# Optimization experiments

Hardware: AMD Instinct MI355X
Metric: run time of the kernel (lower is better)

Reference implementation:

```python
import jax, jax.numpy as jnp
import numpy as np

THRESHOLD = 15.0
INIT_RATIO = 0.5
WINDOW_T = 100
C1 = INIT_RATIO * THRESHOLD            # 7.5, initial membrane potential
C2 = 1.0 / THRESHOLD                   # 1/15
C3 = (1.0 - INIT_RATIO) / WINDOW_T     # 0.005


def snn_layer(spikes, mem, hat_spikes, W, b):
    """One SNNLinear layer in training mode.
    spikes: [T,B,in], mem: [B,out], hat_spikes: [B,in], W: [out,in], b: [out].
    Returns (ss [T,B,out], mem_final [B,out], hat_s [B,out]).
    """
    T = spikes.shape[0]
    # delta_us = fc(spikes): [T,B,out]
    delta_us = jnp.einsum('tbi,oi->tbo', spikes, W) + b

    def step(carry, du):
        m, sum_u = carry
        m = m + du
        s = (m > THRESHOLD).astype(m.dtype)
        m = jnp.clip(m, 0.0, THRESHOLD)
        sum_u = sum_u + m
        m = m - m * s  # reset to 0 where spiked
        return (m, sum_u), s

    (mem_f, sum_u), ss = jax.lax.scan(step, (mem, jnp.zeros_like(mem)), delta_us)
    # In torch this loop runs under no_grad
    ss = jax.lax.stop_gradient(ss)
    mem_f = jax.lax.stop_gradient(mem_f)
    hat_s_fwd = jnp.mean(ss, axis=0)
    hat_u_fwd = jax.lax.stop_gradient(sum_u) / T

    # delta_u = fc(hat_spikes): grad path
    delta_u = hat_spikes @ W.T + b
    # ForwardFirstBackwardSecond: forward value hat_u_fwd, gradient flows to delta_u
    hat_u = hat_u_fwd + (delta_u - jax.lax.stop_gradient(delta_u))
    g = jnp.maximum(hat_u * C2, C3)
    hat_s = hat_s_fwd + (g - jax.lax.stop_gradient(g))
    return ss, mem_f, hat_s


def setup_inputs() -> dict:
    key = jax.random.key(0)
    ks = jax.random.split(key, 8)
    T, B = 50, 256
    shapes = [1024, 2048, 2048, 1024]
    spikes = jax.random.bernoulli(ks[0], 0.1, (T, B, shapes[0])).astype(jnp.float32)
    hat_spk = jax.random.uniform(ks[1], (B, shapes[0]), jnp.float32) * 0.2
    mem0 = jnp.full((B, shapes[1]), C1, jnp.float32)
    mem1 = jnp.full((B, shapes[2]), C1, jnp.float32)
    mem2 = jnp.full((B, shapes[3]), C1, jnp.float32)
    W0 = jax.random.normal(ks[2], (shapes[1], shapes[0]), jnp.float32)
    b0 = jax.random.normal(ks[3], (shapes[1],), jnp.float32)
    W1 = jax.random.normal(ks[4], (shapes[2], shapes[1]), jnp.float32)
    b1 = jax.random.normal(ks[5], (shapes[2],), jnp.float32)
    W2 = jax.random.normal(ks[6], (shapes[3], shapes[2]), jnp.float32)
    b2 = jax.random.normal(ks[7], (shapes[3],), jnp.float32)
    return {"spikes": spikes, "hat_spk": hat_spk, "mem0": mem0, "mem1": mem1,
            "mem2": mem2, "W0": W0, "b0": b0, "W1": W1, "b1": b1, "W2": W2, "b2": b2}


def reference(spikes, hat_spk, mem0, mem1, mem2, W0, b0, W1, b1, W2, b2):
    s, _, h = snn_layer(spikes, mem0, hat_spk, W0, b0)
    s, _, h = snn_layer(s, mem1, h, W1, b1)
    s, _, h = snn_layer(s, mem2, h, W2, b2)
    return s, h
```

## Files before the change

### kernel.cpp

```cpp
#include <hip/hip_runtime.h>
#include <cstdint>
#include <cstddef>

#define T_STEPS 50
#define BATCH   256
#define TC      10
#define TCG     5

__global__ __launch_bounds__(256)
void pack_spikes_k(const float* __restrict__ A, uint32_t* __restrict__ P) {
    const int i    = (int)blockIdx.x * 256 + (int)threadIdx.x;
    const int lane = (int)threadIdx.x & 63;
    const unsigned long long m = __ballot(A[i] != 0.0f);
    if ((lane & 31) == 0)
        P[i >> 5] = (uint32_t)((lane & 32) ? (m >> 32) : m);
}


template<int K, int O>
__global__ __launch_bounds__(256)
void gemm_k(const uint32_t* __restrict__ Ain,
            const float* __restrict__ W,
            const float* __restrict__ bias,
            float* __restrict__ DU)
{
    constexpr int NW = K / 32;
    __shared__ float Wsm[32][256];

    const int tid = (int)threadIdx.x;
    const int o_l = tid & 63;
    const int wid = tid >> 6;
    const int o0  = (int)blockIdx.x * 256;
    const int oq  = o0 + 4 * o_l;
    const int b_u = __builtin_amdgcn_readfirstlane((int)blockIdx.y * 4 + wid);
    const int tc0 = (int)blockIdx.z * TCG;
    const uint32_t* __restrict__ Ab = Ain + (size_t)b_u * NW;

    const float4 bb4 = *(const float4*)(bias + oq);

    float pre[TCG][4], cur[TCG][4];
#pragma unroll
    for (int tt = 0; tt < TCG; ++tt)
#pragma unroll
        for (int c = 0; c < 4; ++c) { pre[tt][c] = 0.0f; cur[tt][c] = 0.0f; }

    for (int wt = 0; wt < NW; ++wt) {
#pragma unroll
        for (int r = 0; r < 8; ++r) {
            const int i    = tid + r * 256;
            const int orow = i >> 3;
            const int q    = i & 7;
            const float4 v = *(const float4*)(W + (size_t)(o0 + orow) * K + wt * 32 + q * 4);
            const int pc   = (((orow >> 2) ^ q) << 2) | (orow & 3);
            Wsm[4 * q + 0][pc] = v.x;
            Wsm[4 * q + 1][pc] = v.y;
            Wsm[4 * q + 2][pc] = v.z;
            Wsm[4 * q + 3][pc] = v.w;
        }
        uint32_t M[TCG];
#pragma unroll
        for (int tt = 0; tt < TCG; ++tt)
            M[tt] = __builtin_amdgcn_readfirstlane(
                        Ab[(size_t)(tc0 + tt) * (BATCH * NW) + wt]);
        __syncthreads();

#pragma unroll 8
        for (int kk = 0; kk < 32; ++kk) {
            const float4 wv = *(const float4*)&Wsm[kk][(o_l ^ ((kk >> 2) & 7)) << 2];
#pragma unroll
            for (int tt = 0; tt < TCG; ++tt) {
                const uint32_t fb = ((M[tt] >> kk) & 1u) ? 0x3f800000u : 0u;
                const float f = __builtin_bit_cast(float, fb);
                cur[tt][0] = __builtin_fmaf(f, wv.x, cur[tt][0]);
                cur[tt][1] = __builtin_fmaf(f, wv.y, cur[tt][1]);
                cur[tt][2] = __builtin_fmaf(f, wv.z, cur[tt][2]);
                cur[tt][3] = __builtin_fmaf(f, wv.w, cur[tt][3]);
            }
        }
        __syncthreads();

        if (((wt + 1) & 15) == 0) {
#pragma unroll
            for (int tt = 0; tt < TCG; ++tt)
#pragma unroll
                for (int c = 0; c < 4; ++c) {
                    pre[tt][c] = pre[tt][c] + cur[tt][c];
                    cur[tt][c] = 0.0f;
                }
        }
    }

#pragma unroll
    for (int tt = 0; tt < TCG; ++tt) {
        const int t = tc0 + tt;
        float4 du;
        du.x = (pre[tt][0] + cur[tt][0]) + bb4.x;
        du.y = (pre[tt][1] + cur[tt][1]) + bb4.y;
        du.z = (pre[tt][2] + cur[tt][2]) + bb4.z;
        du.w = (pre[tt][3] + cur[tt][3]) + bb4.w;
        *(float4*)(DU + (size_t)t * (BATCH * O) + (size_t)b_u * O + oq) = du;
    }
}

template<int O, bool LAST>
__global__ __launch_bounds__(256)
void scan_k(const float* __restrict__ DU,
            const float* __restrict__ mem,
            uint32_t* __restrict__ Pout,
            float* __restrict__ SSout,
            float* __restrict__ Hout)
{
    constexpr int NWO = O / 32;
    __shared__ unsigned char pk[4][64];

    const int tid = (int)threadIdx.x;
    const int o_l = tid & 63;
    const int wid = tid >> 6;
    const int b   = (int)blockIdx.y;
    const int o0  = (int)blockIdx.x * 1024 + wid * 256;
    const int oq  = o0 + 4 * o_l;

    float4 m4 = *(const float4*)(mem + (size_t)b * O + oq);
    int c0 = 0, c1 = 0, c2 = 0, c3 = 0;

    float4 du = *(const float4*)(DU + (size_t)b * O + oq);

    for (int t = 0; t < T_STEPS; ++t) {
        float4 dun;
        if (t + 1 < T_STEPS)
            dun = *(const float4*)(DU + (size_t)(t + 1) * (BATCH * O) + (size_t)b * O + oq);
        m4.x += du.x; m4.y += du.y; m4.z += du.z; m4.w += du.w;
        const bool s0 = m4.x > 15.0f, s1 = m4.y > 15.0f,
                   s2 = m4.z > 15.0f, s3 = m4.w > 15.0f;
        m4.x = fminf(fmaxf(m4.x, 0.0f), 15.0f);
        m4.y = fminf(fmaxf(m4.y, 0.0f), 15.0f);
        m4.z = fminf(fmaxf(m4.z, 0.0f), 15.0f);
        m4.w = fminf(fmaxf(m4.w, 0.0f), 15.0f);
        if (s0) { m4.x = 0.0f; ++c0; }
        if (s1) { m4.y = 0.0f; ++c1; }
        if (s2) { m4.z = 0.0f; ++c2; }
        if (s3) { m4.w = 0.0f; ++c3; }

        if (LAST) {
            *(float4*)(SSout + (size_t)t * (BATCH * O) + (size_t)b * O + oq) =
                make_float4(s0 ? 1.0f : 0.0f, s1 ? 1.0f : 0.0f,
                            s2 ? 1.0f : 0.0f, s3 ? 1.0f : 0.0f);
        } else {
            pk[wid][o_l] = (unsigned char)((s0 ? 1 : 0) | (s1 ? 2 : 0) |
                                           (s2 ? 4 : 0) | (s3 ? 8 : 0));
            __syncthreads();
            if (o_l < 8) {
                const uint2 d = *(const uint2*)&pk[wid][o_l * 8];
                uint32_t x = d.x & 0x0F0F0F0Fu;
                x = (x | (x >> 4)) & 0x00FF00FFu;
                x = (x | (x >> 8)) & 0x0000FFFFu;
                uint32_t y = d.y & 0x0F0F0F0Fu;
                y = (y | (y >> 4)) & 0x00FF00FFu;
                y = (y | (y >> 8)) & 0x0000FFFFu;
                Pout[(size_t)t * (BATCH * NWO) + (size_t)b * NWO + (o0 >> 5) + o_l]
                    = x | (y << 16);
            }
            __syncthreads();
        }
        du = dun;
    }
    if (LAST) {
        *(float4*)(Hout + (size_t)b * O + oq) =
            make_float4((float)c0 / 50.0f, (float)c1 / 50.0f,
                        (float)c2 / 50.0f, (float)c3 / 50.0f);
    }
}

template<int K, int O, bool LAST>
__global__ __launch_bounds__(256)
void snn_k(const uint32_t* __restrict__ Ain,
           const float* __restrict__ W,
           const float* __restrict__ bias,
           const float* __restrict__ mem,
           uint32_t* __restrict__ Pout,
           float* __restrict__ SSout,
           float* __restrict__ Hout)
{
    constexpr int NW  = K / 32;
    constexpr int NWO = O / 32;
    __shared__ float Wsm[32][256];
    __shared__ unsigned char pk[4][64];

    const int tid = (int)threadIdx.x;
    const int o_l = tid & 63;
    const int wid = tid >> 6;
    const int o0  = (int)blockIdx.x * 256;
    const int oq  = o0 + 4 * o_l;
    const int b_u = __builtin_amdgcn_readfirstlane((int)blockIdx.y * 4 + wid);
    const uint32_t* __restrict__ Ab = Ain + (size_t)b_u * NW;

    float4 m4 = *(const float4*)(mem + (size_t)b_u * O + oq);
    const float4 bb4 = *(const float4*)(bias + oq);
    int c0 = 0, c1 = 0, c2 = 0, c3 = 0;

    for (int tc0 = 0; tc0 < T_STEPS; tc0 += TC) {
        float pre[TC][4], cur[TC][4];
#pragma unroll
        for (int tt = 0; tt < TC; ++tt)
#pragma unroll
            for (int c = 0; c < 4; ++c) { pre[tt][c] = 0.0f; cur[tt][c] = 0.0f; }

        for (int wt = 0; wt < NW; ++wt) {
#pragma unroll
            for (int r = 0; r < 8; ++r) {
                const int i    = tid + r * 256;
                const int orow = i >> 3;
                const int q    = i & 7;
                const float4 v = *(const float4*)(W + (size_t)(o0 + orow) * K + wt * 32 + q * 4);
                const int pc   = (((orow >> 2) ^ q) << 2) | (orow & 3);
                Wsm[4 * q + 0][pc] = v.x;
                Wsm[4 * q + 1][pc] = v.y;
                Wsm[4 * q + 2][pc] = v.z;
                Wsm[4 * q + 3][pc] = v.w;
            }
            uint32_t M[TC];
#pragma unroll
            for (int tt = 0; tt < TC; ++tt)
                M[tt] = Ab[(size_t)(tc0 + tt) * (BATCH * NW) + wt];
            __syncthreads();

#pragma unroll 8
            for (int kk = 0; kk < 32; ++kk) {
                const float4 wv = *(const float4*)&Wsm[kk][(o_l ^ ((kk >> 2) & 7)) << 2];
#pragma unroll
                for (int tt = 0; tt < TC; ++tt) {
                    const float f = __builtin_bit_cast(float, ((M[tt] >> kk) & 1u) * 0x3f800000u);
                    cur[tt][0] = __builtin_fmaf(f, wv.x, cur[tt][0]);
                    cur[tt][1] = __builtin_fmaf(f, wv.y, cur[tt][1]);
                    cur[tt][2] = __builtin_fmaf(f, wv.z, cur[tt][2]);
                    cur[tt][3] = __builtin_fmaf(f, wv.w, cur[tt][3]);
                }
            }
            __syncthreads();

            if (((wt + 1) & 15) == 0) {
#pragma unroll
                for (int tt = 0; tt < TC; ++tt)
#pragma unroll
                    for (int c = 0; c < 4; ++c) {
                        pre[tt][c] = pre[tt][c] + cur[tt][c];
                        cur[tt][c] = 0.0f;
                    }
            }
        }

#pragma unroll
        for (int tt = 0; tt < TC; ++tt) {
            const int t = tc0 + tt;
            const float du0 = (pre[tt][0] + cur[tt][0]) + bb4.x;
            const float du1 = (pre[tt][1] + cur[tt][1]) + bb4.y;
            const float du2 = (pre[tt][2] + cur[tt][2]) + bb4.z;
            const float du3 = (pre[tt][3] + cur[tt][3]) + bb4.w;
            m4.x += du0; m4.y += du1; m4.z += du2; m4.w += du3;
            const bool s0 = m4.x > 15.0f, s1 = m4.y > 15.0f,
                       s2 = m4.z > 15.0f, s3 = m4.w > 15.0f;
            m4.x = fminf(fmaxf(m4.x, 0.0f), 15.0f);
            m4.y = fminf(fmaxf(m4.y, 0.0f), 15.0f);
            m4.z = fminf(fmaxf(m4.z, 0.0f), 15.0f);
            m4.w = fminf(fmaxf(m4.w, 0.0f), 15.0f);
            if (s0) { m4.x = 0.0f; ++c0; }
            if (s1) { m4.y = 0.0f; ++c1; }
            if (s2) { m4.z = 0.0f; ++c2; }
            if (s3) { m4.w = 0.0f; ++c3; }

            if (LAST) {
                *(float4*)(SSout + (size_t)t * (BATCH * O) + (size_t)b_u * O + oq) =
                    make_float4(s0 ? 1.0f : 0.0f, s1 ? 1.0f : 0.0f,
                                s2 ? 1.0f : 0.0f, s3 ? 1.0f : 0.0f);
            } else {
                pk[wid][o_l] = (unsigned char)((s0 ? 1 : 0) | (s1 ? 2 : 0) |
                                               (s2 ? 4 : 0) | (s3 ? 8 : 0));
                __syncthreads();
                if (o_l < 8) {
                    const uint2 d = *(const uint2*)&pk[wid][o_l * 8];
                    uint32_t x = d.x & 0x0F0F0F0Fu;
                    x = (x | (x >> 4)) & 0x00FF00FFu;
                    x = (x | (x >> 8)) & 0x0000FFFFu;
                    uint32_t y = d.y & 0x0F0F0F0Fu;
                    y = (y | (y >> 4)) & 0x00FF00FFu;
                    y = (y | (y >> 8)) & 0x0000FFFFu;
                    Pout[(size_t)t * (BATCH * NWO) + (size_t)b_u * NWO + (o0 >> 5) + o_l]
                        = x | (y << 16);
                }
                __syncthreads();
            }
        }
    }
    if (LAST) {
        *(float4*)(Hout + (size_t)b_u * O + oq) =
            make_float4((float)c0 / 50.0f, (float)c1 / 50.0f,
                        (float)c2 / 50.0f, (float)c3 / 50.0f);
    }
}

extern "C" void kernel_launch(void* const* d_in, const int* in_sizes, int n_in,
                              void* d_out, int out_size, void* d_ws, size_t ws_size,
                              hipStream_t stream) {
    (void)out_size;

    const float *spikes = nullptr, *mem0 = nullptr, *mem1 = nullptr, *mem2 = nullptr;
    const float *W0 = nullptr, *b0 = nullptr, *W1 = nullptr, *b1 = nullptr;
    const float *W2 = nullptr, *b2 = nullptr;
    int n2048 = 0, nW02 = 0, nMem = 0, n262k = 0;
    for (int i = 0; i < n_in; ++i) {
        const float* p = (const float*)d_in[i];
        switch (in_sizes[i]) {
            case 13107200: spikes = p; break;
            case 4194304:  W1 = p; break;
            case 1024:     b2 = p; break;
            case 2097152:  if (nW02++ == 0) W0 = p; else W2 = p; break;
            case 2048:     if (n2048++ == 0) b0 = p; else b1 = p; break;
            case 524288:   if (nMem++ == 0) mem0 = p; else mem1 = p; break;
            case 262144:   if (n262k++ == 0) ; else mem2 = p; break;
            default: break;
        }
    }
    if (!spikes || !W0 || !W1 || !W2 || !b0 || !b1 || !b2 || !mem0 || !mem1 || !mem2) {
        spikes = (const float*)d_in[0];
        mem0 = (const float*)d_in[2]; mem1 = (const float*)d_in[3];
        mem2 = (const float*)d_in[4];
        W0 = (const float*)d_in[5]; b0 = (const float*)d_in[6];
        W1 = (const float*)d_in[7]; b1 = (const float*)d_in[8];
        W2 = (const float*)d_in[9]; b2 = (const float*)d_in[10];
    }

    uint32_t* P0 = (uint32_t*)d_ws;
    uint32_t* P1 = (uint32_t*)((char*)d_ws + (2u << 20));
    uint32_t* P2 = (uint32_t*)((char*)d_ws + (6u << 20));
    float*    DU = (float*)((char*)d_ws + (16u << 20));

    float* out_s = (float*)d_out;
    float* out_h = out_s + (size_t)T_STEPS * BATCH * 1024;

    const int n_sp = T_STEPS * BATCH * 1024;
    pack_spikes_k<<<n_sp / 256, 256, 0, stream>>>(spikes, P0);

    const size_t need = (size_t)(16u << 20)
                      + (size_t)T_STEPS * BATCH * 2048 * sizeof(float);

    if (ws_size >= need) {
        gemm_k<1024, 2048><<<dim3(8, 64, T_STEPS / TCG), dim3(256), 0, stream>>>(
            P0, W0, b0, DU);
        scan_k<2048, false><<<dim3(2, BATCH), dim3(256), 0, stream>>>(
            DU, mem0, P1, nullptr, nullptr);
        gemm_k<2048, 2048><<<dim3(8, 64, T_STEPS / TCG), dim3(256), 0, stream>>>(
            P1, W1, b1, DU);
        scan_k<2048, false><<<dim3(2, BATCH), dim3(256), 0, stream>>>(
            DU, mem1, P2, nullptr, nullptr);
        gemm_k<2048, 1024><<<dim3(4, 64, T_STEPS / TCG), dim3(256), 0, stream>>>(
            P2, W2, b2, DU);
        scan_k<1024, true><<<dim3(1, BATCH), dim3(256), 0, stream>>>(
            DU, mem2, nullptr, out_s, out_h);
    } else {
        snn_k<1024, 2048, false><<<dim3(8, 64), dim3(256), 0, stream>>>(
            P0, W0, b0, mem0, P1, nullptr, nullptr);
        snn_k<2048, 2048, false><<<dim3(8, 64), dim3(256), 0, stream>>>(
            P1, W1, b1, mem1, P2, nullptr, nullptr);
        snn_k<2048, 1024, true><<<dim3(4, 64), dim3(256), 0, stream>>>(
            P2, W2, b2, mem2, nullptr, out_s, out_h);
    }
}
```

Before: 3.519 ms.

## Double the GEMM block to eight waves and prefetch next weight tile and spike masks

The gemm kernel now runs 512 threads per block, eight batch rows per block instead of four, so each staged 32x256 weight tile in shared memory is reused by twice as many waves and global weight traffic drops. The next tile's weights and spike bitmasks are loaded into registers during the current tile's compute, overlapping global latency with FMA work. The trade-off is higher register pressure from the prefetch buffers and fewer, larger blocks per CU.

```diff
diff --git a/kernel.cpp b/kernel.cpp
--- a/kernel.cpp
+++ b/kernel.cpp
@@ -18,7 +18,7 @@
 
 
 template<int K, int O>
-__global__ __launch_bounds__(256)
+__global__ __launch_bounds__(512)
 void gemm_k(const uint32_t* __restrict__ Ain,
             const float* __restrict__ W,
             const float* __restrict__ bias,
@@ -32,44 +32,62 @@
     const int wid = tid >> 6;
     const int o0  = (int)blockIdx.x * 256;
     const int oq  = o0 + 4 * o_l;
-    const int b_u = __builtin_amdgcn_readfirstlane((int)blockIdx.y * 4 + wid);
+    const int b_u = __builtin_amdgcn_readfirstlane((int)blockIdx.y * 8 + wid);
     const int tc0 = (int)blockIdx.z * TCG;
     const uint32_t* __restrict__ Ab = Ain + (size_t)b_u * NW;
 
     const float4 bb4 = *(const float4*)(bias + oq);
 
+    const int s_orow0 = tid >> 3;
+    const int s_q     = tid & 7;
+
     float pre[TCG][4], cur[TCG][4];
 #pragma unroll
     for (int tt = 0; tt < TCG; ++tt)
 #pragma unroll
         for (int c = 0; c < 4; ++c) { pre[tt][c] = 0.0f; cur[tt][c] = 0.0f; }
 
+    float4 pf[4];
+#pragma unroll
+    for (int r = 0; r < 4; ++r)
+        pf[r] = *(const float4*)(W + (size_t)(o0 + s_orow0 + r * 64) * K + s_q * 4);
+    uint32_t Mc[TCG], Mn[TCG];
+#pragma unroll
+    for (int tt = 0; tt < TCG; ++tt)
+        Mc[tt] = __builtin_amdgcn_readfirstlane(
+                     Ab[(size_t)(tc0 + tt) * (BATCH * NW) + 0]);
+
     for (int wt = 0; wt < NW; ++wt) {
 #pragma unroll
-        for (int r = 0; r < 8; ++r) {
-            const int i    = tid + r * 256;
-            const int orow = i >> 3;
-            const int q    = i & 7;
-            const float4 v = *(const float4*)(W + (size_t)(o0 + orow) * K + wt * 32 + q * 4);
-            const int pc   = (((orow >> 2) ^ q) << 2) | (orow & 3);
-            Wsm[4 * q + 0][pc] = v.x;
-            Wsm[4 * q + 1][pc] = v.y;
-            Wsm[4 * q + 2][pc] = v.z;
-            Wsm[4 * q + 3][pc] = v.w;
-        }
-        uint32_t M[TCG];
-#pragma unroll
-        for (int tt = 0; tt < TCG; ++tt)
-            M[tt] = __builtin_amdgcn_readfirstlane(
-                        Ab[(size_t)(tc0 + tt) * (BATCH * NW) + wt]);
+        for (int r = 0; r < 4; ++r) {
+            const int orow = s_orow0 + r * 64;
+            const int pc   = (((orow >> 2) ^ s_q) << 2) | (orow & 3);
+            Wsm[4 * s_q + 0][pc] = pf[r].x;
+            Wsm[4 * s_q + 1][pc] = pf[r].y;
+            Wsm[4 * s_q + 2][pc] = pf[r].z;
+            Wsm[4 * s_q + 3][pc] = pf[r].w;
+        }
+        if (wt + 1 < NW) {
+#pragma unroll
+            for (int tt = 0; tt < TCG; ++tt)
+                Mn[tt] = __builtin_amdgcn_readfirstlane(
+                             Ab[(size_t)(tc0 + tt) * (BATCH * NW) + (wt + 1)]);
+        }
         __syncthreads();
+
+        if (wt + 1 < NW) {
+#pragma unroll
+            for (int r = 0; r < 4; ++r)
+                pf[r] = *(const float4*)(W + (size_t)(o0 + s_orow0 + r * 64) * K
+                                           + (wt + 1) * 32 + s_q * 4);
+        }
 
 #pragma unroll 8
         for (int kk = 0; kk < 32; ++kk) {
             const float4 wv = *(const float4*)&Wsm[kk][(o_l ^ ((kk >> 2) & 7)) << 2];
 #pragma unroll
             for (int tt = 0; tt < TCG; ++tt) {
-                const uint32_t fb = ((M[tt] >> kk) & 1u) ? 0x3f800000u : 0u;
+                const uint32_t fb = ((Mc[tt] >> kk) & 1u) ? 0x3f800000u : 0u;
                 const float f = __builtin_bit_cast(float, fb);
                 cur[tt][0] = __builtin_fmaf(f, wv.x, cur[tt][0]);
                 cur[tt][1] = __builtin_fmaf(f, wv.y, cur[tt][1]);
@@ -78,6 +96,10 @@
             }
         }
         __syncthreads();
+
+#pragma unroll
+        for (int tt = 0; tt < TCG; ++tt)
+            Mc[tt] = Mn[tt];
 
         if (((wt + 1) & 15) == 0) {
 #pragma unroll
@@ -344,15 +366,15 @@
                       + (size_t)T_STEPS * BATCH * 2048 * sizeof(float);
 
     if (ws_size >= need) {
-        gemm_k<1024, 2048><<<dim3(8, 64, T_STEPS / TCG), dim3(256), 0, stream>>>(
+        gemm_k<1024, 2048><<<dim3(8, 32, T_STEPS / TCG), dim3(512), 0, stream>>>(
             P0, W0, b0, DU);
         scan_k<2048, false><<<dim3(2, BATCH), dim3(256), 0, stream>>>(
             DU, mem0, P1, nullptr, nullptr);
-        gemm_k<2048, 2048><<<dim3(8, 64, T_STEPS / TCG), dim3(256), 0, stream>>>(
+        gemm_k<2048, 2048><<<dim3(8, 32, T_STEPS / TCG), dim3(512), 0, stream>>>(
             P1, W1, b1, DU);
         scan_k<2048, false><<<dim3(2, BATCH), dim3(256), 0, stream>>>(
             DU, mem1, P2, nullptr, nullptr);
-        gemm_k<2048, 1024><<<dim3(4, 64, T_STEPS / TCG), dim3(256), 0, stream>>>(
+        gemm_k<2048, 1024><<<dim3(4, 32, T_STEPS / TCG), dim3(512), 0, stream>>>(
             P2, W2, b2, DU);
         scan_k<1024, true><<<dim3(1, BATCH), dim3(256), 0, stream>>>(
             DU, mem2, nullptr, out_s, out_h);
```

New measurement: 3.274 ms. 7.0% less time.
